# Kernel optimization log

Hardware: AMD Instinct MI355X
Metric: run time of the kernel (lower is better)

Reference implementation:

```python
import jax, jax.numpy as jnp
import numpy as np

B, NQ, NK, C, OUT = 4, 2048, 2048, 4, 64
H = 16          # hidden size of the radial MLP (hardcoded in MlpRBF)
WINDOW = 0.25   # window_size default in MlpRBF


def setup_inputs() -> dict:
    key = jax.random.key(0)
    ks = jax.random.split(key, 20)
    s = 0.5
    return {
        "key_pos": jax.random.uniform(ks[0], (B, NK, 1), dtype=jnp.float32),
        "queries": jax.random.uniform(ks[1], (B, NQ, 1), dtype=jnp.float32),
        "values": jax.random.normal(ks[2], (B, NK, 1), dtype=jnp.float32),
        "key_chan": jax.random.randint(ks[3], (B, NK), 0, C),
        # radial MLP: 1 -> 16 -> 16 -> 16 -> 1, ReLU hidden activations
        "w0": jax.random.normal(ks[4], (H, 1)) * s, "b0": jax.random.normal(ks[5], (H,)) * 0.1,
        "w1": jax.random.normal(ks[6], (H, H)) * (s / np.sqrt(H)), "b1": jax.random.normal(ks[7], (H,)) * 0.1,
        "w2": jax.random.normal(ks[8], (H, H)) * (s / np.sqrt(H)), "b2": jax.random.normal(ks[9], (H,)) * 0.1,
        "w3": jax.random.normal(ks[10], (1, H)) * (s / np.sqrt(H)), "b3": jax.random.normal(ks[11], (1,)) * 0.1,
        # density_transform: Linear(1,1)
        "wd": jax.random.normal(ks[12], (1, 1)) * s, "bd": jax.random.normal(ks[13], (1,)) * 0.1,
        # resizer: Linear(2*C, OUT)
        "wr": jax.random.normal(ks[14], (OUT, 2 * C)) * (s / np.sqrt(2 * C)), "br": jax.random.normal(ks[15], (OUT,)) * 0.1,
    }


def reference(key_pos, queries, values, key_chan,
              w0, b0, w1, b1, w2, b2, w3, b3, wd, bd, wr, br):
    # pairwise |key - query| distances: [B, NQ, NK] (is_abs_dist=True)
    diff = jnp.abs(key_pos[:, None, :, 0] - queries[:, :, None, 0])
    window = diff < WINDOW                              # [B, NQ, NK] bool

    # per-pair radial MLP (x_dim=1 input, 3 hidden layers of 16, scalar out)
    x = diff[..., None]                                 # [B, NQ, NK, 1]
    h = jax.nn.relu(x @ w0.T + b0)
    h = jax.nn.relu(h @ w1.T + b1)
    h = jax.nn.relu(h @ w2.T + b2)
    raw = (h @ w3.T + b3)[..., 0]                       # [B, NQ, NK]
    weight = jnp.abs(raw) * window.astype(raw.dtype)    # mask_and_apply + abs + window mask

    # per-channel masked reduction (equivalent to gathering keys of each channel)
    onehot = jax.nn.one_hot(key_chan, C, dtype=weight.dtype)      # [B, NK, C]
    density = jnp.einsum('bqk,bkc->bqc', weight, onehot)          # [B, NQ, C]
    numer = jnp.einsum('bqk,bkc->bqc', weight, onehot * values)   # values: [B, NK, 1]
    targets = numer / (density + 1e-5)                            # normalized weighted sum

    # density channel: sigmoid(Linear(density*0.1 - 1))
    dens_feat = jax.nn.sigmoid((density * 0.1 - 1.0) * wd[0, 0] + bd[0])

    # per-channel SetConv output is cat([target, density]) -> interleave: [t0,d0,t1,d1,...]
    feat = jnp.stack([targets, dens_feat], axis=-1).reshape(targets.shape[0], targets.shape[1], 2 * C)
    return feat @ wr.T + br                             # [B, NQ, OUT]
```

## Files before the change

kernel.cpp:

```cpp
#include <hip/hip_runtime.h>
#include <math.h>

constexpr int B_  = 4;
constexpr int NQ_ = 2048;
constexpr int NK_ = 2048;
constexpr int C_  = 4;
constexpr int OUT_ = 64;
constexpr int H_  = 16;
constexpr float WINDOW_ = 0.25f;

constexpr int   TAB_   = 4096;
constexpr float SCALE_ = TAB_ / WINDOW_;
constexpr int   QT_    = 8;
constexpr int   SLOT_  = 1024;
constexpr int   NBIN_  = 16;
constexpr float SENT_  = 4e9f;

constexpr size_t OFF_TAB  = 0;
constexpr size_t OFF_SORT = 16384;
constexpr size_t OFF_BINS = 16384 + 16 * SLOT_ * 8;

__global__ __launch_bounds__(256) void preprocess(
    const float* __restrict__ key_pos,
    const float* __restrict__ values,
    const int*   __restrict__ key_chan,
    const float* __restrict__ w0, const float* __restrict__ b0,
    const float* __restrict__ w1, const float* __restrict__ b1,
    const float* __restrict__ w2, const float* __restrict__ b2,
    const float* __restrict__ w3, const float* __restrict__ b3,
    float* __restrict__ tab,
    float2* __restrict__ sorted,
    int*    __restrict__ bins)
{
    const int tid = threadIdx.x;

    if (blockIdx.x < 16) {
        const int i = blockIdx.x * 256 + tid;
        const float x = ((float)i + 0.5f) * (1.0f / SCALE_);
        float h[H_], g[H_];
        #pragma unroll
        for (int j = 0; j < H_; ++j)
            h[j] = fmaxf(fmaf(x, w0[j], b0[j]), 0.f);
        #pragma unroll
        for (int j = 0; j < H_; ++j) {
            float a = b1[j];
            #pragma unroll
            for (int k = 0; k < H_; ++k) a = fmaf(w1[j * H_ + k], h[k], a);
            g[j] = fmaxf(a, 0.f);
        }
        #pragma unroll
        for (int j = 0; j < H_; ++j) {
            float a = b2[j];
            #pragma unroll
            for (int k = 0; k < H_; ++k) a = fmaf(w2[j * H_ + k], g[k], a);
            h[j] = fmaxf(a, 0.f);
        }
        float a = b3[0];
        #pragma unroll
        for (int k = 0; k < H_; ++k) a = fmaf(w3[k], h[k], a);
        tab[i] = fabsf(a);
        return;
    }

    const int slot = blockIdx.x - 16;
    const int b    = slot >> 2;
    const int c    = slot & 3;

    __shared__ int   hist[NBIN_ + 1];
    __shared__ int   ofs [NBIN_];
    __shared__ float lpos[SLOT_];
    __shared__ float lval[SLOT_];

    if (tid <= NBIN_) hist[tid] = 0;
    __syncthreads();

    const float* kp = key_pos  + b * NK_;
    const float* vv = values   + b * NK_;
    const int*   cc = key_chan + b * NK_;

    for (int i = tid; i < NK_; i += 256) {
        if (cc[i] == c) {
            const int bin = min((int)(kp[i] * (float)NBIN_), NBIN_ - 1);
            atomicAdd(&hist[bin], 1);
        }
    }
    __syncthreads();

    if (tid == 0) {
        int run = 0;
        #pragma unroll
        for (int t = 0; t < NBIN_; ++t) {
            const int h = hist[t];
            hist[t] = run; ofs[t] = run; run += h;
        }
        hist[NBIN_] = run;
    }
    __syncthreads();

    const int cnt = hist[NBIN_];
    if (tid <= NBIN_) bins[slot * (NBIN_ + 1) + tid] = hist[tid];

    for (int i = tid; i < NK_; i += 256) {
        if (cc[i] == c) {
            const float p   = kp[i];
            const int   bin = min((int)(p * (float)NBIN_), NBIN_ - 1);
            const int   idx = atomicAdd(&ofs[bin], 1);
            lpos[idx] = p; lval[idx] = vv[i];
        }
    }
    __syncthreads();

    for (int i = tid; i < SLOT_; i += 256)
        sorted[slot * SLOT_ + i] =
            (i < cnt) ? make_float2(lpos[i], lval[i]) : make_float2(SENT_, 0.f);
}

__global__ __launch_bounds__(256) void setconv_main(
    const float*  __restrict__ queries,
    const float2* __restrict__ sorted,
    const int*    __restrict__ bins,
    const float*  __restrict__ tab,
    const float*  __restrict__ wd, const float* __restrict__ bd,
    const float*  __restrict__ wr, const float* __restrict__ br,
    float* __restrict__ out)
{
    __shared__ __align__(16) float ltab[TAB_];

    const int tid = threadIdx.x;

    {
        const float4* t4 = (const float4*)tab;
        float4*       l4 = (float4*)ltab;
        #pragma unroll
        for (int i = 0; i < TAB_ / 4 / 256; ++i)
            l4[i * 256 + tid] = t4[i * 256 + tid];
    }
    __syncthreads();

    const int blk  = blockIdx.x;
    const int b    = blk >> 8;
    const int tile = blk & 255;
    const int wave = tid >> 6;
    const int lane = tid & 63;

    const float wd0 = wd[0];
    const float bd0 = bd[0];

    float wrow[8];
    #pragma unroll
    for (int j = 0; j < 8; ++j) wrow[j] = wr[lane * 8 + j];
    const float brv = br[lane];

    #pragma unroll
    for (int qq = 0; qq < 2; ++qq) {
        const int   qi   = tile * QT_ + wave * 2 + qq;
        const float qpos = queries[b * NQ_ + qi];

        int lo_bin = (int)floorf((qpos - WINDOW_) * (float)NBIN_);
        lo_bin = (lo_bin < 0) ? 0 : ((lo_bin > NBIN_) ? NBIN_ : lo_bin);
        int hi_bin = (int)ceilf((qpos + WINDOW_) * (float)NBIN_);
        hi_bin = (hi_bin < 0) ? 0 : ((hi_bin > NBIN_) ? NBIN_ : hi_bin);

        float dens[4], num[4];
        #pragma unroll
        for (int c = 0; c < 4; ++c) {
            const int slot = b * 4 + c;
            const int* bs  = bins + slot * (NBIN_ + 1);
            const int lo = bs[lo_bin] & ~63;
            const int hi = bs[hi_bin];
            const float2* seg = sorted + slot * SLOT_;

            float d = 0.f, n = 0.f;
            for (int k = lo; k < hi; k += 64) {
                const float2 pv = seg[k + lane];
                const float dd  = fabsf(pv.x - qpos);
                const float t   = fminf(dd * SCALE_, (float)(TAB_ - 1));
                const float tv  = ltab[(int)t];
                const float w   = (dd < WINDOW_) ? tv : 0.f;
                d += w;
                n  = fmaf(w, pv.y, n);
            }
            dens[c] = d; num[c] = n;
        }

        #pragma unroll
        for (int off = 32; off >= 1; off >>= 1) {
            #pragma unroll
            for (int c = 0; c < 4; ++c) {
                dens[c] += __shfl_xor(dens[c], off, 64);
                num [c] += __shfl_xor(num [c], off, 64);
            }
        }

        float acc = brv;
        #pragma unroll
        for (int c = 0; c < 4; ++c) {
            const float tgt = num[c] / (dens[c] + 1e-5f);
            const float x   = (dens[c] * 0.1f - 1.0f) * wd0 + bd0;
            const float df  = 1.0f / (1.0f + expf(-x));
            acc = fmaf(wrow[2 * c],     tgt, acc);
            acc = fmaf(wrow[2 * c + 1], df,  acc);
        }
        out[(b * NQ_ + qi) * OUT_ + lane] = acc;
    }
}

extern "C" void kernel_launch(void* const* d_in, const int* in_sizes, int n_in,
                              void* d_out, int out_size, void* d_ws, size_t ws_size,
                              hipStream_t stream) {
    (void)in_sizes; (void)n_in; (void)out_size; (void)ws_size;

    char* ws = (char*)d_ws;
    float*  tab    = (float*) (ws + OFF_TAB);
    float2* sorted = (float2*)(ws + OFF_SORT);
    int*    bins   = (int*)   (ws + OFF_BINS);

    preprocess<<<dim3(32), dim3(256), 0, stream>>>(
        (const float*)d_in[0],
        (const float*)d_in[2],
        (const int*)  d_in[3],
        (const float*)d_in[4],  (const float*)d_in[5],
        (const float*)d_in[6],  (const float*)d_in[7],
        (const float*)d_in[8],  (const float*)d_in[9],
        (const float*)d_in[10], (const float*)d_in[11],
        tab, sorted, bins);

    setconv_main<<<dim3(B_ * (NQ_ / QT_)), dim3(256), 0, stream>>>(
        (const float*)d_in[1],
        sorted, bins, tab,
        (const float*)d_in[12], (const float*)d_in[13],
        (const float*)d_in[14], (const float*)d_in[15],
        (float*)d_out);
}
```

Measured before the change: 109.1 us.

## Use one query per wave, finer bins, and interleave channel loads with prefetch

```diff
diff --git a/kernel.cpp b/kernel.cpp
--- a/kernel.cpp
+++ b/kernel.cpp
@@ -11,9 +11,9 @@
 
 constexpr int   TAB_   = 4096;
 constexpr float SCALE_ = TAB_ / WINDOW_;
-constexpr int   QT_    = 8;
+constexpr int   QW_    = 4;
 constexpr int   SLOT_  = 1024;
-constexpr int   NBIN_  = 16;
+constexpr int   NBIN_  = 64;
 constexpr float SENT_  = 4e9f;
 
 constexpr size_t OFF_TAB  = 0;
@@ -115,7 +115,7 @@
             (i < cnt) ? make_float2(lpos[i], lval[i]) : make_float2(SENT_, 0.f);
 }
 
-__global__ __launch_bounds__(256) void setconv_main(
+__global__ __launch_bounds__(256, 8) void setconv_main(
     const float*  __restrict__ queries,
     const float2* __restrict__ sorted,
     const int*    __restrict__ bins,
@@ -138,71 +138,86 @@
     __syncthreads();
 
     const int blk  = blockIdx.x;
-    const int b    = blk >> 8;
-    const int tile = blk & 255;
+    const int b    = blk >> 9;
+    const int tile = blk & 511;
     const int wave = tid >> 6;
     const int lane = tid & 63;
 
+    const int   qi   = tile * QW_ + wave;
+    const float qpos = queries[b * NQ_ + qi];
+
+    int lo_bin = (int)floorf((qpos - WINDOW_) * (float)NBIN_);
+    lo_bin = (lo_bin < 0) ? 0 : ((lo_bin > NBIN_) ? NBIN_ : lo_bin);
+    int hi_bin = (int)ceilf((qpos + WINDOW_) * (float)NBIN_);
+    hi_bin = (hi_bin < 0) ? 0 : ((hi_bin > NBIN_) ? NBIN_ : hi_bin);
+
+    int k[4];
+    const float2* seg[4];
+    int rounds = 0;
+    #pragma unroll
+    for (int c = 0; c < 4; ++c) {
+        const int slot = b * 4 + c;
+        const int* bs  = bins + slot * (NBIN_ + 1);
+        k[c] = bs[lo_bin];
+        const int span = bs[hi_bin] - k[c];
+        const int rc   = (span + 63) >> 6;
+        rounds = (rc > rounds) ? rc : rounds;
+        seg[c] = sorted + slot * SLOT_;
+    }
+
+    float dens[4] = {0.f, 0.f, 0.f, 0.f};
+    float num [4] = {0.f, 0.f, 0.f, 0.f};
+
+    float2 cur[4];
+    #pragma unroll
+    for (int c = 0; c < 4; ++c)
+        cur[c] = seg[c][min(k[c], SLOT_ - 64) + lane];
+
+    for (int r = 0; r < rounds; ++r) {
+        float2 nxt[4];
+        #pragma unroll
+        for (int c = 0; c < 4; ++c)
+            nxt[c] = seg[c][min(k[c] + 64, SLOT_ - 64) + lane];
+
+        #pragma unroll
+        for (int c = 0; c < 4; ++c) {
+            const float dd = fabsf(cur[c].x - qpos);
+            const float t  = fminf(dd * SCALE_, (float)(TAB_ - 1));
+            const float tv = ltab[(int)t];
+            const float w  = (dd < WINDOW_) ? tv : 0.f;
+            dens[c] += w;
+            num [c]  = fmaf(w, cur[c].y, num[c]);
+        }
+
+        #pragma unroll
+        for (int c = 0; c < 4; ++c) { cur[c] = nxt[c]; k[c] += 64; }
+    }
+
+    #pragma unroll
+    for (int off = 32; off >= 1; off >>= 1) {
+        #pragma unroll
+        for (int c = 0; c < 4; ++c) {
+            dens[c] += __shfl_xor(dens[c], off, 64);
+            num [c] += __shfl_xor(num [c], off, 64);
+        }
+    }
+
     const float wd0 = wd[0];
     const float bd0 = bd[0];
-
     float wrow[8];
     #pragma unroll
     for (int j = 0; j < 8; ++j) wrow[j] = wr[lane * 8 + j];
-    const float brv = br[lane];
-
-    #pragma unroll
-    for (int qq = 0; qq < 2; ++qq) {
-        const int   qi   = tile * QT_ + wave * 2 + qq;
-        const float qpos = queries[b * NQ_ + qi];
-
-        int lo_bin = (int)floorf((qpos - WINDOW_) * (float)NBIN_);
-        lo_bin = (lo_bin < 0) ? 0 : ((lo_bin > NBIN_) ? NBIN_ : lo_bin);
-        int hi_bin = (int)ceilf((qpos + WINDOW_) * (float)NBIN_);
-        hi_bin = (hi_bin < 0) ? 0 : ((hi_bin > NBIN_) ? NBIN_ : hi_bin);
-
-        float dens[4], num[4];
-        #pragma unroll
-        for (int c = 0; c < 4; ++c) {
-            const int slot = b * 4 + c;
-            const int* bs  = bins + slot * (NBIN_ + 1);
-            const int lo = bs[lo_bin] & ~63;
-            const int hi = bs[hi_bin];
-            const float2* seg = sorted + slot * SLOT_;
-
-            float d = 0.f, n = 0.f;
-            for (int k = lo; k < hi; k += 64) {
-                const float2 pv = seg[k + lane];
-                const float dd  = fabsf(pv.x - qpos);
-                const float t   = fminf(dd * SCALE_, (float)(TAB_ - 1));
-                const float tv  = ltab[(int)t];
-                const float w   = (dd < WINDOW_) ? tv : 0.f;
-                d += w;
-                n  = fmaf(w, pv.y, n);
-            }
-            dens[c] = d; num[c] = n;
-        }
-
-        #pragma unroll
-        for (int off = 32; off >= 1; off >>= 1) {
-            #pragma unroll
-            for (int c = 0; c < 4; ++c) {
-                dens[c] += __shfl_xor(dens[c], off, 64);
-                num [c] += __shfl_xor(num [c], off, 64);
-            }
-        }
-
-        float acc = brv;
-        #pragma unroll
-        for (int c = 0; c < 4; ++c) {
-            const float tgt = num[c] / (dens[c] + 1e-5f);
-            const float x   = (dens[c] * 0.1f - 1.0f) * wd0 + bd0;
-            const float df  = 1.0f / (1.0f + expf(-x));
-            acc = fmaf(wrow[2 * c],     tgt, acc);
-            acc = fmaf(wrow[2 * c + 1], df,  acc);
-        }
-        out[(b * NQ_ + qi) * OUT_ + lane] = acc;
-    }
+    float acc = br[lane];
+
+    #pragma unroll
+    for (int c = 0; c < 4; ++c) {
+        const float tgt = num[c] / (dens[c] + 1e-5f);
+        const float x   = (dens[c] * 0.1f - 1.0f) * wd0 + bd0;
+        const float df  = 1.0f / (1.0f + expf(-x));
+        acc = fmaf(wrow[2 * c],     tgt, acc);
+        acc = fmaf(wrow[2 * c + 1], df,  acc);
+    }
+    out[(b * NQ_ + qi) * OUT_ + lane] = acc;
 }
 
 extern "C" void kernel_launch(void* const* d_in, const int* in_sizes, int n_in,
@@ -225,7 +240,7 @@
         (const float*)d_in[10], (const float*)d_in[11],
         tab, sorted, bins);
 
-    setconv_main<<<dim3(B_ * (NQ_ / QT_)), dim3(256), 0, stream>>>(
+    setconv_main<<<dim3(B_ * (NQ_ / QW_)), dim3(256), 0, stream>>>(
         (const float*)d_in[1],
         sorted, bins, tab,
         (const float*)d_in[12], (const float*)d_in[13],
```

Measured after the change: 101.4 us. -7.0%, faster.
